# Performance work log

Hardware: AMD Instinct MI355X
Metric: run time of the kernel (lower is better)

Reference implementation:

```python
import jax, jax.numpy as jnp
import numpy as np

DIM = 1024
NUM_HEADS = 16
HEAD_DIM = DIM // NUM_HEADS
SCALE = HEAD_DIM ** -0.5
B, LQ, LK = 2, 2048, 2048


def setup_inputs() -> dict:
    key = jax.random.key(0)
    ks = jax.random.split(key, 12)
    init = 1.0 / np.sqrt(DIM)  # ~ torch Linear default scale
    inp = {
        "q": jax.random.normal(ks[0], (B, LQ, DIM), jnp.float32),
        "k": jax.random.normal(ks[1], (B, LK, DIM), jnp.float32),
        "v": jax.random.normal(ks[2], (B, LK, DIM), jnp.float32),
        "kv_mask": jnp.ones((B, LK), jnp.int32),
        "Wq": jax.random.uniform(ks[3], (DIM, DIM), jnp.float32, -init, init),
        "bq": jax.random.uniform(ks[4], (DIM,), jnp.float32, -init, init),
        "Wk": jax.random.uniform(ks[5], (DIM, DIM), jnp.float32, -init, init),
        "bk": jax.random.uniform(ks[6], (DIM,), jnp.float32, -init, init),
        "Wv": jax.random.uniform(ks[7], (DIM, DIM), jnp.float32, -init, init),
        "bv": jax.random.uniform(ks[8], (DIM,), jnp.float32, -init, init),
        "Wo": jax.random.uniform(ks[9], (DIM, DIM), jnp.float32, -init, init),
        "bo": jax.random.uniform(ks[10], (DIM,), jnp.float32, -init, init),
    }
    return inp


def reference(q, k, v, kv_mask, Wq, bq, Wk, bk, Wv, bv, Wo, bo):
    Bq, Lq, D = q.shape
    Lk = k.shape[1]
    H, Hd = NUM_HEADS, HEAD_DIM
    # projections (torch Linear: x @ W.T + b); split heads -> [B, H, L, Hd]
    qh = (q @ Wq.T + bq).reshape(Bq, Lq, H, Hd).transpose(0, 2, 1, 3)
    kh = (k @ Wk.T + bk).reshape(Bq, Lk, H, Hd).transpose(0, 2, 1, 3)
    vh = (v @ Wv.T + bv).reshape(Bq, Lk, H, Hd).transpose(0, 2, 1, 3)
    # scores [B, H, Lq, Lk]
    attn = jnp.einsum("bhqd,bhkd->bhqk", qh, kh) * SCALE
    mask = (kv_mask != 0)[:, None, None, :]
    attn = jnp.where(mask, attn, -jnp.inf)
    attn = jax.nn.softmax(attn, axis=-1)
    # dropout is identity at inference (p applied only in train mode)
    out = jnp.einsum("bhqk,bhkd->bhqd", attn, vh)
    out = out.transpose(0, 2, 1, 3).reshape(Bq, Lq, D)
    return out @ Wo.T + bo
```

## Files before the change

kernel.cpp:

```cpp
#include <hip/hip_runtime.h>
#include <stdint.h>

typedef unsigned short u16;
typedef __attribute__((ext_vector_type(8))) __bf16 bf16x8;
typedef __attribute__((ext_vector_type(4))) float f32x4;

#define DIM 1024
#define NH 16
#define HD 64
#define BSZ 2
#define LQ 2048
#define LK 2048
#define SCALE_LOG2E 0.18033688011112043f
#define MNEG -3.0e38f


static __device__ __forceinline__ float b2f(u16 u) {
  union { uint32_t i; float f; } v; v.i = ((uint32_t)u) << 16; return v.f;
}
static __device__ __forceinline__ u16 f2b(float f) {
  uint32_t x = __float_as_uint(f);
  return (u16)((x + 0x7fffu + ((x >> 16) & 1u)) >> 16);
}
static __device__ __forceinline__ uint32_t pk2r(float lo, float hi) {
  uint32_t a = __float_as_uint(lo) + 0x8000u;
  uint32_t b = __float_as_uint(hi) + 0x8000u;
  return __builtin_amdgcn_perm(b, a, 0x07060302u);
}
static __device__ __forceinline__ f32x4 zero4() {
  f32x4 z; z[0] = 0.f; z[1] = 0.f; z[2] = 0.f; z[3] = 0.f; return z;
}
static __device__ __forceinline__ float exp2c(float s) {
  return exp2f(fminf(s, 30.0f));
}
static __device__ __forceinline__ void gload_lds16(const u16* g, u16* l) {
  __builtin_amdgcn_global_load_lds(
      (const __attribute__((address_space(1))) void*)g,
      (__attribute__((address_space(3))) void*)l, 16, 0, 0);
}

__global__ void mask_allvalid(const int* __restrict__ kvmask, int* allv) {
  int b = blockIdx.x;
  int base = b * LK + threadIdx.x * 8;
  int ok = 1;
#pragma unroll
  for (int j = 0; j < 8; ++j) ok &= (kvmask[base + j] != 0);
  unsigned long long m = __ballot(ok != 0);
  if ((threadIdx.x & 63) == 0 && m != ~0ULL) atomicAnd(&allv[b], 0);
}

struct ConvArgs {
  const float* src[11];
  long long cum[12];
  u16* dst;
};

__global__ void convert_inputs(ConvArgs ca) {
  long long c = (long long)blockIdx.x * blockDim.x + threadIdx.x;
  long long e0 = c * 8;
  if (e0 >= ca.cum[11]) return;
  int s = 0;
  while (e0 >= ca.cum[s + 1]) ++s;
  const float* sp = ca.src[s] + (e0 - ca.cum[s]);
  union { uint4 v; uint32_t w[4]; } t;
#pragma unroll
  for (int j = 0; j < 4; ++j) t.w[j] = pk2r(sp[2 * j], sp[2 * j + 1]);
  *(uint4*)(ca.dst + e0) = t.v;
}

struct GemmArgs {
  const u16* X[3];
  const u16* W[3];
  const u16* Bias[3];
  void* Y[3];
  float osc[3];
  int f32out;
  int vtz;
};

__global__ __launch_bounds__(256, 2) void gemm_bt_bias(GemmArgs ga) {
  const int K = DIM, N = DIM;
  __shared__ u16 smem[17408];
  u16* const Al = smem;
  u16* const Bl = smem + 8192;
  const int tid = threadIdx.x;
  const int wave = tid >> 6, lane = tid & 63;
  const int wm = wave >> 1, wn = wave & 1;
  const int lrow = lane & 15, quad = lane >> 4;
  const int z = blockIdx.z;
  const u16* X = ga.X[z];
  const u16* W = ga.W[z];
  const u16* Bias = ga.Bias[z];
  const float osc = ga.osc[z];
  const int m0 = blockIdx.x * 128;
  const int n0 = blockIdx.y * 128;

  f32x4 acc[4][4];
#pragma unroll
  for (int i = 0; i < 4; ++i)
#pragma unroll
    for (int j = 0; j < 4; ++j) acc[i][j] = zero4();

  const int cbase = wave * 256;
  for (int k0 = 0; k0 < K; k0 += 64) {
    __syncthreads();
#pragma unroll
    for (int i = 0; i < 4; ++i) {
      int c = cbase + i * 64 + lane;
      int row = c >> 3, colb = c & 7;
      gload_lds16(X + (size_t)(m0 + row) * K + k0 + colb * 8,
                  &Al[(cbase + i * 64) * 8]);
      gload_lds16(W + (size_t)(n0 + row) * K + k0 + colb * 8,
                  &Bl[(cbase + i * 64) * 8]);
    }
    __syncthreads();
#pragma unroll
    for (int ks = 0; ks < 2; ++ks) {
      bf16x8 af[4], bfr[4];
#pragma unroll
      for (int t = 0; t < 4; ++t)
        af[t] = *(const bf16x8*)&Al[(wm * 64 + t * 16 + lrow) * 64 + ks * 32 + quad * 8];
#pragma unroll
      for (int t = 0; t < 4; ++t)
        bfr[t] = *(const bf16x8*)&Bl[(wn * 64 + t * 16 + lrow) * 64 + ks * 32 + quad * 8];
#pragma unroll
      for (int mt = 0; mt < 4; ++mt)
#pragma unroll
        for (int nt = 0; nt < 4; ++nt)
          acc[mt][nt] = __builtin_amdgcn_mfma_f32_16x16x32_bf16(af[mt], bfr[nt], acc[mt][nt], 0, 0, 0);
    }
  }

  if (z == ga.vtz) {
    u16* Yv = (u16*)ga.Y[z];
    u16* const VT = smem;
    __syncthreads();
#pragma unroll
    for (int nt = 0; nt < 4; ++nt) {
      int colL = wn * 64 + nt * 16 + lrow;
      float bv = b2f(Bias[n0 + colL]);
#pragma unroll
      for (int mt = 0; mt < 4; ++mt) {
        int keyL = wm * 64 + mt * 16 + quad * 4;
        uint2 w;
        w.x = pk2r((acc[mt][nt][0] + bv) * osc, (acc[mt][nt][1] + bv) * osc);
        w.y = pk2r((acc[mt][nt][2] + bv) * osc, (acc[mt][nt][3] + bv) * osc);
        *(uint2*)&VT[colL * 136 + keyL] = w;
      }
    }
    __syncthreads();
    const int bb = m0 >> 11, key0 = m0 & 2047;
#pragma unroll
    for (int i = 0; i < 8; ++i) {
      int c = i * 256 + tid;
      int colL = c >> 4, k8 = c & 15;
      int hh = (n0 + colL) >> 6, dd = (n0 + colL) & 63;
      *(uint4*)(Yv + ((size_t)(bb * NH + hh) * HD + dd) * LK + key0 + k8 * 8) =
          *(const uint4*)&VT[colL * 136 + k8 * 8];
    }
  } else if (ga.f32out) {
    float* Yf = (float*)ga.Y[z];
#pragma unroll
    for (int nt = 0; nt < 4; ++nt) {
      int col = n0 + wn * 64 + nt * 16 + lrow;
      float bv = b2f(Bias[col]);
#pragma unroll
      for (int mt = 0; mt < 4; ++mt) {
        int rowb = m0 + wm * 64 + mt * 16 + quad * 4;
#pragma unroll
        for (int r = 0; r < 4; ++r)
          Yf[(size_t)(rowb + r) * N + col] = (acc[mt][nt][r] + bv) * osc;
      }
    }
  } else {
    u16* Yv = (u16*)ga.Y[z];
#pragma unroll
    for (int nt = 0; nt < 4; ++nt) {
      int col = n0 + wn * 64 + nt * 16 + lrow;
      float bv = b2f(Bias[col]);
#pragma unroll
      for (int mt = 0; mt < 4; ++mt) {
        int rowb = m0 + wm * 64 + mt * 16 + quad * 4;
#pragma unroll
        for (int r = 0; r < 4; ++r)
          Yv[(size_t)(rowb + r) * N + col] = f2b((acc[mt][nt][r] + bv) * osc);
      }
    }
  }
}

__global__ __launch_bounds__(256, 2) void attn_fused(
    const u16* __restrict__ qp, const u16* __restrict__ kp,
    const u16* __restrict__ vpt, const int* __restrict__ kvmask,
    const int* __restrict__ allv, u16* __restrict__ op) {
  __shared__ u16 Kl[128 * 72];
  __shared__ u16 Vt[64 * 136];
  __shared__ u16 Pq[4][32 * 136];
  __shared__ float Ml[128];
  const int tid = threadIdx.x;
  const int wave = tid >> 6, lane = tid & 63;
  const int lrow = lane & 15, quad = lane >> 4;
  const int bh = blockIdx.y;
  const int b = bh >> 4, h = bh & 15;
  const int q0 = blockIdx.x * 128;
  const bool av = (allv[b] != 0);

  const u16* qbase = qp + (size_t)b * LQ * DIM + h * HD;
  const u16* kbase = kp + (size_t)b * LK * DIM + h * HD;
  const u16* vtb = vpt + (size_t)(b * NH + h) * HD * LK;
  const int* mbase = kvmask + b * LK;
  const int wq0 = q0 + wave * 32;

  bf16x8 qf[2][2];
#pragma unroll
  for (int mt = 0; mt < 2; ++mt)
#pragma unroll
    for (int ks = 0; ks < 2; ++ks)
      qf[mt][ks] = *(const bf16x8*)(qbase + (size_t)(wq0 + mt * 16 + lrow) * DIM + ks * 32 + quad * 8);

  f32x4 acco[2][4];
  float lsum[2];
#pragma unroll
  for (int mt = 0; mt < 2; ++mt) {
#pragma unroll
    for (int dt = 0; dt < 4; ++dt) acco[mt][dt] = zero4();
    lsum[mt] = 0.0f;
  }

  for (int kc = 0; kc < LK; kc += 128) {
    __syncthreads();
#pragma unroll
    for (int i = 0; i < 4; ++i) {
      int c = i * 256 + tid;
      int row = c >> 3, colb = c & 7;
      *(uint4*)&Kl[row * 72 + colb * 8] =
          *(const uint4*)(kbase + (size_t)(kc + row) * DIM + colb * 8);
      int d = c >> 4, k8 = c & 15;
      *(uint4*)&Vt[d * 136 + k8 * 8] =
          *(const uint4*)(vtb + (size_t)d * LK + kc + k8 * 8);
    }
    if (!av && tid < 128) Ml[tid] = mbase[kc + tid] ? 0.0f : MNEG;
    __syncthreads();

    f32x4 sacc[2][8];
#pragma unroll
    for (int mt = 0; mt < 2; ++mt)
#pragma unroll
      for (int nt = 0; nt < 8; ++nt) sacc[mt][nt] = zero4();
#pragma unroll
    for (int ks = 0; ks < 2; ++ks) {
#pragma unroll
      for (int nt = 0; nt < 8; ++nt) {
        bf16x8 kf = *(const bf16x8*)&Kl[(nt * 16 + lrow) * 72 + ks * 32 + quad * 8];
        sacc[0][nt] = __builtin_amdgcn_mfma_f32_16x16x32_bf16(kf, qf[0][ks], sacc[0][nt], 0, 0, 0);
        sacc[1][nt] = __builtin_amdgcn_mfma_f32_16x16x32_bf16(kf, qf[1][ks], sacc[1][nt], 0, 0, 0);
      }
    }

    u16* pqw = &Pq[wave][0];
#pragma unroll
    for (int mt = 0; mt < 2; ++mt) {
      float rsum = 0.0f;
      u16* prow = &pqw[(mt * 16 + lrow) * 136];
      if (av) {
#pragma unroll
        for (int nt = 0; nt < 8; ++nt) {
          float p0 = exp2c(sacc[mt][nt][0]);
          float p1 = exp2c(sacc[mt][nt][1]);
          float p2 = exp2c(sacc[mt][nt][2]);
          float p3 = exp2c(sacc[mt][nt][3]);
          rsum += (p0 + p1) + (p2 + p3);
          uint2 w; w.x = pk2r(p0, p1); w.y = pk2r(p2, p3);
          *(uint2*)&prow[nt * 16 + quad * 4] = w;
        }
      } else {
#pragma unroll
        for (int nt = 0; nt < 8; ++nt) {
          f32x4 mq = *(const f32x4*)&Ml[nt * 16 + quad * 4];
          float p0 = exp2c(sacc[mt][nt][0] + mq[0]);
          float p1 = exp2c(sacc[mt][nt][1] + mq[1]);
          float p2 = exp2c(sacc[mt][nt][2] + mq[2]);
          float p3 = exp2c(sacc[mt][nt][3] + mq[3]);
          rsum += (p0 + p1) + (p2 + p3);
          uint2 w; w.x = pk2r(p0, p1); w.y = pk2r(p2, p3);
          *(uint2*)&prow[nt * 16 + quad * 4] = w;
        }
      }
      rsum += __shfl_xor(rsum, 16);
      rsum += __shfl_xor(rsum, 32);
      lsum[mt] += rsum;
    }

#pragma unroll
    for (int kb = 0; kb < 4; ++kb) {
      bf16x8 pf0 = *(const bf16x8*)&pqw[(0 * 16 + lrow) * 136 + kb * 32 + quad * 8];
      bf16x8 pf1 = *(const bf16x8*)&pqw[(1 * 16 + lrow) * 136 + kb * 32 + quad * 8];
#pragma unroll
      for (int dt = 0; dt < 4; ++dt) {
        bf16x8 vf = *(const bf16x8*)&Vt[(dt * 16 + lrow) * 136 + kb * 32 + quad * 8];
        acco[0][dt] = __builtin_amdgcn_mfma_f32_16x16x32_bf16(vf, pf0, acco[0][dt], 0, 0, 0);
        acco[1][dt] = __builtin_amdgcn_mfma_f32_16x16x32_bf16(vf, pf1, acco[1][dt], 0, 0, 0);
      }
    }
  }

  u16* ob = op + (size_t)b * LQ * DIM + h * HD;
#pragma unroll
  for (int mt = 0; mt < 2; ++mt) {
    float inv = lsum[mt] > 0.0f ? 1.0f / lsum[mt] : 0.0f;
    int q = wq0 + mt * 16 + lrow;
#pragma unroll
    for (int dt = 0; dt < 4; ++dt) {
      uint2 w;
      w.x = pk2r(acco[mt][dt][0] * inv, acco[mt][dt][1] * inv);
      w.y = pk2r(acco[mt][dt][2] * inv, acco[mt][dt][3] * inv);
      *(uint2*)&ob[(size_t)q * DIM + dt * 16 + quad * 4] = w;
    }
  }
}

extern "C" void kernel_launch(void* const* d_in, const int* in_sizes, int n_in,
                              void* d_out, int out_size, void* d_ws, size_t ws_size,
                              hipStream_t stream) {
  (void)in_sizes; (void)n_in; (void)out_size; (void)ws_size;
  const int* kvmask = (const int*)d_in[3];

  u16* ws = (u16*)d_ws;
  const long long SQ = (long long)BSZ * LQ * DIM;
  const long long SW = (long long)DIM * DIM;
  const long long SB = DIM;
  long long cum[12];
  cum[0] = 0;
  cum[1] = cum[0] + SQ;
  cum[2] = cum[1] + SQ;
  cum[3] = cum[2] + SQ;
  cum[4] = cum[3] + SW;
  cum[5] = cum[4] + SW;
  cum[6] = cum[5] + SW;
  cum[7] = cum[6] + SW;
  cum[8] = cum[7] + SB;
  cum[9] = cum[8] + SB;
  cum[10] = cum[9] + SB;
  cum[11] = cum[10] + SB;
  const long long canon_end = cum[11];
  u16* cq  = ws + cum[0];
  u16* ck  = ws + cum[1];
  u16* cv  = ws + cum[2];
  u16* cWq = ws + cum[3];
  u16* cWk = ws + cum[4];
  u16* cWv = ws + cum[5];
  u16* cWo = ws + cum[6];
  u16* cbq = ws + cum[7];
  u16* cbk = ws + cum[8];
  u16* cbv = ws + cum[9];
  u16* cbo = ws + cum[10];
  u16* qp  = ws + canon_end;
  u16* kp  = qp + SQ;
  u16* vpt = kp + SQ;
  u16* ao  = vpt + SQ;
  int* allv = (int*)(ao + SQ);

  hipMemsetAsync(allv, 0xFF, 2 * sizeof(int), stream);
  mask_allvalid<<<BSZ, 256, 0, stream>>>(kvmask, allv);

  ConvArgs ca;
  ca.src[0] = (const float*)d_in[0];
  ca.src[1] = (const float*)d_in[1];
  ca.src[2] = (const float*)d_in[2];
  ca.src[3] = (const float*)d_in[4];
  ca.src[4] = (const float*)d_in[6];
  ca.src[5] = (const float*)d_in[8];
  ca.src[6] = (const float*)d_in[10];
  ca.src[7] = (const float*)d_in[5];
  ca.src[8] = (const float*)d_in[7];
  ca.src[9] = (const float*)d_in[9];
  ca.src[10] = (const float*)d_in[11];
  for (int i = 0; i < 12; ++i) ca.cum[i] = cum[i];
  ca.dst = ws;
  int conv_blocks = (int)((canon_end / 8 + 255) / 256);
  convert_inputs<<<conv_blocks, 256, 0, stream>>>(ca);

  const int M = BSZ * LQ;

  GemmArgs g1;
  g1.X[0] = cq; g1.W[0] = cWq; g1.Bias[0] = cbq; g1.Y[0] = qp;
  g1.X[1] = ck; g1.W[1] = cWk; g1.Bias[1] = cbk; g1.Y[1] = kp;
  g1.X[2] = cv; g1.W[2] = cWv; g1.Bias[2] = cbv; g1.Y[2] = vpt;
  g1.osc[0] = SCALE_LOG2E;
  g1.osc[1] = 1.0f;
  g1.osc[2] = 1.0f;
  g1.f32out = 0;
  g1.vtz = 2;
  gemm_bt_bias<<<dim3(M / 128, DIM / 128, 3), dim3(256), 0, stream>>>(g1);

  attn_fused<<<dim3(LQ / 128, BSZ * NH), dim3(256), 0, stream>>>(qp, kp, vpt, kvmask, allv, ao);

  GemmArgs g2;
  g2.X[0] = ao; g2.W[0] = cWo; g2.Bias[0] = cbo; g2.Y[0] = d_out;
  g2.X[1] = ao; g2.W[1] = cWo; g2.Bias[1] = cbo; g2.Y[1] = d_out;
  g2.X[2] = ao; g2.W[2] = cWo; g2.Bias[2] = cbo; g2.Y[2] = d_out;
  g2.osc[0] = 1.0f; g2.osc[1] = 1.0f; g2.osc[2] = 1.0f;
  g2.f32out = 1;
  g2.vtz = -1;
  gemm_bt_bias<<<dim3(M / 128, DIM / 128, 1), dim3(256), 0, stream>>>(g2);
}
```

Before: 265.0 us.

## Register-prefetch next K/V tile, shrink P buffer, defer row-sum reduction

```diff
diff --git a/kernel.cpp b/kernel.cpp
--- a/kernel.cpp
+++ b/kernel.cpp
@@ -189,13 +189,13 @@
   }
 }
 
-__global__ __launch_bounds__(256, 2) void attn_fused(
+__global__ __launch_bounds__(256, 3) void attn_fused(
     const u16* __restrict__ qp, const u16* __restrict__ kp,
     const u16* __restrict__ vpt, const int* __restrict__ kvmask,
     const int* __restrict__ allv, u16* __restrict__ op) {
   __shared__ u16 Kl[128 * 72];
   __shared__ u16 Vt[64 * 136];
-  __shared__ u16 Pq[4][32 * 136];
+  __shared__ u16 Pp[4][32 * 40];
   __shared__ float Ml[128];
   const int tid = threadIdx.x;
   const int wave = tid >> 6, lane = tid & 63;
@@ -227,19 +227,23 @@
     lsum[mt] = 0.0f;
   }
 
+  const int kr_row = tid >> 3, kr_cb = (tid & 7) * 8;
+  const int vr_d = tid >> 4, vr_k8 = (tid & 15) * 8;
+  uint4 kr[4], vr[4];
+
+#pragma unroll
+  for (int i = 0; i < 4; ++i) {
+    kr[i] = *(const uint4*)(kbase + (size_t)(i * 32 + kr_row) * DIM + kr_cb);
+    vr[i] = *(const uint4*)(vtb + (size_t)(i * 16 + vr_d) * LK + vr_k8);
+  }
+#pragma unroll
+  for (int i = 0; i < 4; ++i) {
+    *(uint4*)&Kl[(i * 32 + kr_row) * 72 + kr_cb] = kr[i];
+    *(uint4*)&Vt[(i * 16 + vr_d) * 136 + vr_k8] = vr[i];
+  }
+  if (!av && tid < 128) Ml[tid] = mbase[tid] ? 0.0f : MNEG;
+
   for (int kc = 0; kc < LK; kc += 128) {
-    __syncthreads();
-#pragma unroll
-    for (int i = 0; i < 4; ++i) {
-      int c = i * 256 + tid;
-      int row = c >> 3, colb = c & 7;
-      *(uint4*)&Kl[row * 72 + colb * 8] =
-          *(const uint4*)(kbase + (size_t)(kc + row) * DIM + colb * 8);
-      int d = c >> 4, k8 = c & 15;
-      *(uint4*)&Vt[d * 136 + k8 * 8] =
-          *(const uint4*)(vtb + (size_t)d * LK + kc + k8 * 8);
-    }
-    if (!av && tid < 128) Ml[tid] = mbase[kc + tid] ? 0.0f : MNEG;
     __syncthreads();
 
     f32x4 sacc[2][8];
@@ -257,44 +261,52 @@
       }
     }
 
-    u16* pqw = &Pq[wave][0];
-#pragma unroll
-    for (int mt = 0; mt < 2; ++mt) {
-      float rsum = 0.0f;
-      u16* prow = &pqw[(mt * 16 + lrow) * 136];
-      if (av) {
-#pragma unroll
-        for (int nt = 0; nt < 8; ++nt) {
-          float p0 = exp2c(sacc[mt][nt][0]);
-          float p1 = exp2c(sacc[mt][nt][1]);
-          float p2 = exp2c(sacc[mt][nt][2]);
-          float p3 = exp2c(sacc[mt][nt][3]);
-          rsum += (p0 + p1) + (p2 + p3);
-          uint2 w; w.x = pk2r(p0, p1); w.y = pk2r(p2, p3);
-          *(uint2*)&prow[nt * 16 + quad * 4] = w;
+    const bool more = (kc + 128) < LK;
+    if (more) {
+#pragma unroll
+      for (int i = 0; i < 4; ++i) {
+        kr[i] = *(const uint4*)(kbase + (size_t)(kc + 128 + i * 32 + kr_row) * DIM + kr_cb);
+        vr[i] = *(const uint4*)(vtb + (size_t)(i * 16 + vr_d) * LK + (kc + 128) + vr_k8);
+      }
+    }
+
+    u16* pqw = &Pp[wave][0];
+#pragma unroll
+    for (int kb = 0; kb < 4; ++kb) {
+#pragma unroll
+      for (int mt = 0; mt < 2; ++mt) {
+        float rsum = 0.0f;
+        u16* prow = &pqw[(mt * 16 + lrow) * 40];
+        if (av) {
+#pragma unroll
+          for (int ntl = 0; ntl < 2; ++ntl) {
+            const int nt = 2 * kb + ntl;
+            float p0 = exp2c(sacc[mt][nt][0]);
+            float p1 = exp2c(sacc[mt][nt][1]);
+            float p2 = exp2c(sacc[mt][nt][2]);
+            float p3 = exp2c(sacc[mt][nt][3]);
+            rsum += (p0 + p1) + (p2 + p3);
+            uint2 w; w.x = pk2r(p0, p1); w.y = pk2r(p2, p3);
+            *(uint2*)&prow[ntl * 16 + quad * 4] = w;
+          }
+        } else {
+#pragma unroll
+          for (int ntl = 0; ntl < 2; ++ntl) {
+            const int nt = 2 * kb + ntl;
+            f32x4 mq = *(const f32x4*)&Ml[nt * 16 + quad * 4];
+            float p0 = exp2c(sacc[mt][nt][0] + mq[0]);
+            float p1 = exp2c(sacc[mt][nt][1] + mq[1]);
+            float p2 = exp2c(sacc[mt][nt][2] + mq[2]);
+            float p3 = exp2c(sacc[mt][nt][3] + mq[3]);
+            rsum += (p0 + p1) + (p2 + p3);
+            uint2 w; w.x = pk2r(p0, p1); w.y = pk2r(p2, p3);
+            *(uint2*)&prow[ntl * 16 + quad * 4] = w;
+          }
         }
-      } else {
-#pragma unroll
-        for (int nt = 0; nt < 8; ++nt) {
-          f32x4 mq = *(const f32x4*)&Ml[nt * 16 + quad * 4];
-          float p0 = exp2c(sacc[mt][nt][0] + mq[0]);
-          float p1 = exp2c(sacc[mt][nt][1] + mq[1]);
-          float p2 = exp2c(sacc[mt][nt][2] + mq[2]);
-          float p3 = exp2c(sacc[mt][nt][3] + mq[3]);
-          rsum += (p0 + p1) + (p2 + p3);
-          uint2 w; w.x = pk2r(p0, p1); w.y = pk2r(p2, p3);
-          *(uint2*)&prow[nt * 16 + quad * 4] = w;
-        }
-      }
-      rsum += __shfl_xor(rsum, 16);
-      rsum += __shfl_xor(rsum, 32);
-      lsum[mt] += rsum;
-    }
-
-#pragma unroll
-    for (int kb = 0; kb < 4; ++kb) {
-      bf16x8 pf0 = *(const bf16x8*)&pqw[(0 * 16 + lrow) * 136 + kb * 32 + quad * 8];
-      bf16x8 pf1 = *(const bf16x8*)&pqw[(1 * 16 + lrow) * 136 + kb * 32 + quad * 8];
+        lsum[mt] += rsum;
+      }
+      bf16x8 pf0 = *(const bf16x8*)&pqw[(0 * 16 + lrow) * 40 + quad * 8];
+      bf16x8 pf1 = *(const bf16x8*)&pqw[(1 * 16 + lrow) * 40 + quad * 8];
 #pragma unroll
       for (int dt = 0; dt < 4; ++dt) {
         bf16x8 vf = *(const bf16x8*)&Vt[(dt * 16 + lrow) * 136 + kb * 32 + quad * 8];
@@ -302,12 +314,25 @@
         acco[1][dt] = __builtin_amdgcn_mfma_f32_16x16x32_bf16(vf, pf1, acco[1][dt], 0, 0, 0);
       }
     }
+
+    __syncthreads();
+    if (more) {
+#pragma unroll
+      for (int i = 0; i < 4; ++i) {
+        *(uint4*)&Kl[(i * 32 + kr_row) * 72 + kr_cb] = kr[i];
+        *(uint4*)&Vt[(i * 16 + vr_d) * 136 + vr_k8] = vr[i];
+      }
+      if (!av && tid < 128) Ml[tid] = mbase[kc + 128 + tid] ? 0.0f : MNEG;
+    }
   }
 
   u16* ob = op + (size_t)b * LQ * DIM + h * HD;
 #pragma unroll
   for (int mt = 0; mt < 2; ++mt) {
-    float inv = lsum[mt] > 0.0f ? 1.0f / lsum[mt] : 0.0f;
+    float t = lsum[mt];
+    t += __shfl_xor(t, 16);
+    t += __shfl_xor(t, 32);
+    float inv = t > 0.0f ? 1.0f / t : 0.0f;
     int q = wq0 + mt * 16 + lrow;
 #pragma unroll
     for (int dt = 0; dt < 4; ++dt) {
```

After: 318.1 us. 1.2x slower.
